# Optimization experiments

Hardware: AMD Instinct MI355X
Metric: run time of the kernel (lower is better)

## Reference

```python
import jax, jax.numpy as jnp
import numpy as np

N, F, H, L = 1536, 32, 64, 3  # num_nodes, num_features, hidden, num_layers
NEG_SLOPE = 0.01
BN_EPS = 1e-5


def _lrelu(x):
    return jnp.where(x >= 0, x, NEG_SLOPE * x)


def _gin_layer(x, src, tgt, eps, w1, b1, w2, b2, g, be):
    # scatter-add aggregation: out[tgt] += x[src] (source_to_target flow)
    agg = jax.ops.segment_sum(x[src], tgt, num_segments=N)
    h = (1.0 + eps) * x + agg
    h = jax.nn.relu(h @ w1 + b1)
    h = jax.nn.relu(h @ w2 + b2)
    # BatchNorm1d, training-mode (batch statistics, biased variance)
    mean = jnp.mean(h, axis=0)
    var = jnp.mean((h - mean) ** 2, axis=0)
    return (h - mean) * jax.lax.rsqrt(var + BN_EPS) * g + be


def setup_inputs() -> dict:
    key = jax.random.key(0)
    ks = iter(jax.random.split(key, 40))

    def rn(shape, scale=0.05):
        return jax.random.normal(next(ks), shape, dtype=jnp.float32) * scale

    inp = {
        "x": rn((N, F), 1.0),
        "node_features": rn((N, F), 1.0),
        # conv1: F -> H
        "c1_eps": jnp.zeros((), jnp.float32),
        "c1_w1": rn((F, H)), "c1_b1": jnp.zeros((H,), jnp.float32),
        "c1_w2": rn((H, H)), "c1_b2": jnp.zeros((H,), jnp.float32),
        "c1_g": jnp.ones((H,), jnp.float32), "c1_be": jnp.zeros((H,), jnp.float32),
        # L-1 additional GIN convs: H -> H (stacked)
        "cv_eps": jnp.zeros((L - 1,), jnp.float32),
        "cv_w1": rn((L - 1, H, H)), "cv_b1": jnp.zeros((L - 1, H), jnp.float32),
        "cv_w2": rn((L - 1, H, H)), "cv_b2": jnp.zeros((L - 1, H), jnp.float32),
        "cv_g": jnp.ones((L - 1, H), jnp.float32), "cv_be": jnp.zeros((L - 1, H), jnp.float32),
        # projection head
        "lin1_w": rn((H, H)), "lin1_b": jnp.zeros((H,), jnp.float32),
        "lin2_w": rn((H, F)), "lin2_b": jnp.zeros((F,), jnp.float32),
        # edge predictor: 2F -> H -> H -> H -> 1
        "ep_w1": rn((2 * F, H)), "ep_b1": jnp.zeros((H,), jnp.float32),
        "ep_w2": rn((H, H)), "ep_b2": jnp.zeros((H,), jnp.float32),
        "ep_w3": rn((H, H)), "ep_b3": jnp.zeros((H,), jnp.float32),
        "ep_w4": rn((H, 1)), "ep_b4": jnp.zeros((1,), jnp.float32),
    }
    return inp


def reference(x, node_features, c1_eps, c1_w1, c1_b1, c1_w2, c1_b2, c1_g, c1_be,
              cv_eps, cv_w1, cv_b1, cv_w2, cv_b2, cv_g, cv_be,
              lin1_w, lin1_b, lin2_w, lin2_b,
              ep_w1, ep_b1, ep_w2, ep_b2, ep_w3, ep_b3, ep_w4, ep_b4):
    # complete-graph upper-triangular edge list (matches torch.combinations order)
    src, tgt = jnp.triu_indices(N, k=1)
    h = node_features  # forward ignores input x
    xinit = h
    h = _lrelu(_gin_layer(h, src, tgt, c1_eps, c1_w1, c1_b1, c1_w2, c1_b2, c1_g, c1_be))
    for i in range(L - 1):
        h = _lrelu(_gin_layer(h, src, tgt, cv_eps[i], cv_w1[i], cv_b1[i],
                              cv_w2[i], cv_b2[i], cv_g[i], cv_be[i]))
    h = _lrelu(h @ lin1_w + lin1_b)
    h = _lrelu(h @ lin2_w + lin2_b)
    h = h + xinit  # [N, F]

    # edge predictor: gather -> MLP -> sigmoid over E edges
    ef = jnp.concatenate([h[src], h[tgt]], axis=-1)  # [E, 2F]
    e = jax.nn.relu(ef @ ep_w1 + ep_b1)
    e = jax.nn.relu(e @ ep_w2 + ep_b2)
    e = jax.nn.relu(e @ ep_w3 + ep_b3)
    e = jax.nn.sigmoid(e @ ep_w4 + ep_b4)[:, 0]  # [E]

    probs = jnp.zeros((N, N), dtype=h.dtype)
    probs = probs.at[src, tgt].set(e).at[tgt, src].set(e)
    return probs
```

## Files before the change

kernel.cpp:

```cpp
#include <hip/hip_runtime.h>
#include <math.h>

#define NN 1536
#define FF 32
#define HH 64
#define EE (NN*(NN-1)/2)
#define EBLK 2493
#define BN_EPS 1e-5f
#define SLOPE 0.01f

typedef _Float16 v8h   __attribute__((ext_vector_type(8)));
typedef __fp16   v2hf  __attribute__((ext_vector_type(2)));
typedef float    f32x4 __attribute__((ext_vector_type(4)));

union V8H { v8h v; v2hf h2[4]; float4 f4; };

__device__ __forceinline__ float lrelu_f(float v){ return v >= 0.f ? v : SLOPE*v; }

__global__ __launch_bounds__(256) void k_first(
    const float* __restrict__ nf, float* __restrict__ H,
    const float* __restrict__ pw2, const float* __restrict__ pw3,
    _Float16* __restrict__ pwf) {
  int bid = blockIdx.x, tid = threadIdx.x;
  if (bid >= 96) {
    int i = (bid - 96)*256 + tid;
    if (i < 8192) {
      int mat = i >> 12, r = i & 4095;
      int k = r >> 6, cout = r & 63;
      int m = cout >> 4, cc = cout & 15;
      int q, g, b;
      if (mat == 0) { q = k >> 5; g = (k >> 3) & 3; b = k & 7; }
      else { int mF = k >> 4; g = (k >> 2) & 3; int rr = k & 3; q = mF >> 1; b = ((mF & 1) << 2) | rr; }
      const float* W = mat ? pw3 : pw2;
      pwf[mat*4096 + ((q*4 + m)*64 + (g*16 + cc))*8 + b] = (_Float16)W[r];
    }
    return;
  }
  __shared__ float part[8][32];
  int c = tid & 31, y = tid >> 5;
  float s = nf[(bid*16 + y)*32 + c] + nf[(bid*16 + y + 8)*32 + c];
  part[y][c] = s;
  __syncthreads();
  if (y == 0) {
    float S = 0.f;
#pragma unroll
    for (int r = 0; r < 8; ++r) S += part[r][c];
    H[bid*64 + c] = S;
  }
}

__global__ __launch_bounds__(256) void k_bn(
    const float* __restrict__ z, const float* __restrict__ P,
    const float* __restrict__ gg, const float* __restrict__ be,
    float* __restrict__ hbuf, float* __restrict__ H) {
  __shared__ float sums[2][128];
  __shared__ float scl[64], sft[64];
  __shared__ float part[4][64];
  int tid = threadIdx.x, bid = blockIdx.x;
  {
    int c2 = tid & 127, half = tid >> 7;
    float S0 = 0.f, S1 = 0.f;
    int j0 = half*48;
    for (int j = j0; j < j0 + 48; j += 2) { S0 += P[j*128 + c2]; S1 += P[(j+1)*128 + c2]; }
    sums[half][c2] = S0 + S1;
  }
  __syncthreads();
  if (tid < 64) {
    float S = sums[0][tid] + sums[1][tid];
    float Q = sums[0][64 + tid] + sums[1][64 + tid];
    float m  = S * (1.f/NN);
    float iv = rsqrtf(Q * (1.f/NN) - m*m + BN_EPS);
    float sc = iv * gg[tid];
    scl[tid] = sc;
    sft[tid] = be[tid] - m*sc;
  }
  __syncthreads();
  int c = tid & 63, y = tid >> 6;
  float sc = scl[c], sh = sft[c];
  float hs = 0.f;
#pragma unroll
  for (int i = 0; i < 4; ++i) {
    int rr = y + 4*i;
    float h = lrelu_f(z[(bid*16 + rr)*64 + c]*sc + sh);
    hbuf[(bid*16 + rr)*64 + c] = h;
    hs += h;
  }
  part[y][c] = hs;
  __syncthreads();
  if (y == 0)
    H[bid*64 + c] = part[0][c] + part[1][c] + part[2][c] + part[3][c];
}

template<int DIN>
__global__ __launch_bounds__(512) void k_mmp(
    const float* __restrict__ hb, const float* __restrict__ H,
    const float* __restrict__ eps_p,
    const float* __restrict__ W1, const float* __restrict__ b1,
    const float* __restrict__ W2, const float* __restrict__ b2,
    float* __restrict__ zout, float* __restrict__ P) {
  __shared__ float W1s[DIN*64];
  __shared__ float W2s[4096];
  __shared__ float red[8][64];
  __shared__ float pf[64];
  __shared__ float hh[16][DIN];
  __shared__ float uls[16*DIN];
  __shared__ float t1s[16][64];
  __shared__ float pp[8][64], pq[8][64];
  int tid = threadIdx.x, bid = blockIdx.x;
  int c = tid & 63, y = tid >> 6;
  for (int i = tid; i < DIN*64; i += 512) W1s[i] = W1[i];
  for (int i = tid; i < 4096; i += 512)   W2s[i] = W2[i];

  {
    float s = 0.f;
    if (c < DIN) for (int j = y; j < bid; j += 8) s += H[j*64 + c];
    red[y][c] = s;
  }
  if (c < DIN) {
    hh[y][c]     = hb[(bid*16 + y)*DIN + c];
    hh[y + 8][c] = hb[(bid*16 + y + 8)*DIN + c];
  }
  __syncthreads();
  if (y == 0 && c < DIN) {
    float S = 0.f;
#pragma unroll
    for (int r = 0; r < 8; ++r) S += red[r][c];
    pf[c] = S;
  }
  __syncthreads();

  float e1 = 1.f + eps_p[0];
  if (c < DIN) {
    for (int rr = y; rr < 16; rr += 8) {
      float run = pf[c];
      for (int r2 = 0; r2 < rr; ++r2) run += hh[r2][c];
      uls[rr*DIN + c] = e1*hh[rr][c] + run;
    }
  }
  __syncthreads();

  float a0 = b1[c], a1 = a0;
  for (int k = 0; k < DIN; ++k) {
    float w = W1s[k*64 + c];
    a0 = fmaf(uls[y*DIN + k],       w, a0);
    a1 = fmaf(uls[(y + 8)*DIN + k], w, a1);
  }
  t1s[y][c]     = fmaxf(a0, 0.f);
  t1s[y + 8][c] = fmaxf(a1, 0.f);
  __syncthreads();

  float z0 = b2[c], z1 = z0;
  for (int k = 0; k < 64; ++k) {
    float w = W2s[k*64 + c];
    z0 = fmaf(t1s[y][k],     w, z0);
    z1 = fmaf(t1s[y + 8][k], w, z1);
  }
  z0 = fmaxf(z0, 0.f); z1 = fmaxf(z1, 0.f);
  zout[(bid*16 + y)*64 + c]     = z0;
  zout[(bid*16 + y + 8)*64 + c] = z1;

  pp[y][c] = z0 + z1;
  pq[y][c] = z0*z0 + z1*z1;
  __syncthreads();
  if (y == 0) {
    float S = 0.f, Q = 0.f;
#pragma unroll
    for (int r = 0; r < 8; ++r) { S += pp[r][c]; Q += pq[r][c]; }
    P[bid*128 + c]      = S;
    P[bid*128 + 64 + c] = Q;
  }
}

__global__ __launch_bounds__(512) void k_head2(
    const float* __restrict__ z, const float* __restrict__ P,
    const float* __restrict__ gg, const float* __restrict__ be,
    const float* __restrict__ l1w, const float* __restrict__ l1b,
    const float* __restrict__ l2w, const float* __restrict__ l2b,
    const float* __restrict__ nf,
    const float* __restrict__ epw1, const float* __restrict__ epb1,
    _Float16* __restrict__ Ah, _Float16* __restrict__ Bh) {
  __shared__ float W1s[4096];
  __shared__ float W2s[2048];
  __shared__ float Was[2048];
  __shared__ float Wbs[2048];
  __shared__ float sums[4][128];
  __shared__ float scratch[4096];
  __shared__ float scl[64], sft[64];
  int tid = threadIdx.x, c = tid & 63, y = tid >> 6;
  for (int i = tid; i < 4096; i += 512) W1s[i] = l1w[i];
  for (int i = tid; i < 2048; i += 512) { W2s[i] = l2w[i]; Was[i] = epw1[i]; Wbs[i] = epw1[2048 + i]; }

  {
    int c2 = tid & 127, q = tid >> 7;
    float S = 0.f;
    for (int j = q*24; j < q*24 + 24; ++j) S += P[j*128 + c2];
    sums[q][c2] = S;
  }
  __syncthreads();
  if (tid < 64) {
    float S = sums[0][tid] + sums[1][tid] + sums[2][tid] + sums[3][tid];
    float Q = sums[0][64+tid] + sums[1][64+tid] + sums[2][64+tid] + sums[3][64+tid];
    float m  = S * (1.f/NN);
    float iv = rsqrtf(Q * (1.f/NN) - m*m + BN_EPS);
    float sc = iv * gg[tid];
    scl[tid] = sc;
    sft[tid] = be[tid] - m*sc;
  }
  __syncthreads();

  float* t0 = scratch;
  float* t1 = scratch + 1024;
  float* t2 = scratch + 2048;
  int r0 = blockIdx.x*16;

  for (int rr = y; rr < 16; rr += 8)
    t0[rr*64 + c] = lrelu_f(z[(r0 + rr)*64 + c]*scl[c] + sft[c]);
  __syncthreads();
  {
    float a0 = l1b[c], a1 = a0;
    for (int k = 0; k < 64; ++k) {
      float w = W1s[k*64 + c];
      a0 = fmaf(t0[y*64 + k],       w, a0);
      a1 = fmaf(t0[(y + 8)*64 + k], w, a1);
    }
    t1[y*64 + c]       = lrelu_f(a0);
    t1[(y + 8)*64 + c] = lrelu_f(a1);
  }
  __syncthreads();
  if (c < 32) {
    float v0 = l2b[c], v1 = v0;
    for (int k = 0; k < 64; ++k) {
      float w = W2s[k*32 + c];
      v0 = fmaf(t1[y*64 + k],       w, v0);
      v1 = fmaf(t1[(y + 8)*64 + k], w, v1);
    }
    t2[y*32 + c]       = lrelu_f(v0) + nf[(r0 + y)*32 + c];
    t2[(y + 8)*32 + c] = lrelu_f(v1) + nf[(r0 + y + 8)*32 + c];
  }
  __syncthreads();
  {
    float av0 = epb1[c], av1 = av0;
    float bv0 = 0.f, bv1 = 0.f;
    for (int k = 0; k < 32; ++k) {
      float wa = Was[k*64 + c], wb = Wbs[k*64 + c];
      av0 = fmaf(t2[y*32 + k], wa, av0);       bv0 = fmaf(t2[y*32 + k], wb, bv0);
      av1 = fmaf(t2[(y + 8)*32 + k], wa, av1); bv1 = fmaf(t2[(y + 8)*32 + k], wb, bv1);
    }
    Ah[(r0 + y)*64 + c]     = (_Float16)av0;  Bh[(r0 + y)*64 + c]     = (_Float16)bv0;
    Ah[(r0 + y + 8)*64 + c] = (_Float16)av1;  Bh[(r0 + y + 8)*64 + c] = (_Float16)bv1;
  }
}

__global__ __launch_bounds__(256, 3) void k_edges_f16(
    const _Float16* __restrict__ Ah, const _Float16* __restrict__ Bh,
    const _Float16* __restrict__ Wf,
    const float* __restrict__ b2, const float* __restrict__ b3,
    const float* __restrict__ w4, const float* __restrict__ b4,
    float* __restrict__ out) {
  __shared__ _Float16 Wl[8192];
  int tid = threadIdx.x, wid = tid >> 6, lane = tid & 63;
  int c = lane & 15, g = lane >> 4;

  {
    const float4* src = (const float4*)Wf;
    float4* dst = (float4*)Wl;
    for (int i = tid; i < 1024; i += 256) dst[i] = src[i];
  }

  int w = blockIdx.x*4 + wid;
  int cum, kk, sbase;
  if (w < 1524) { cum = 0; kk = 12; sbase = 0; }
  else {
    cum = 1524; kk = 11; sbase = 127;
    while (kk > 1 && w >= cum + 128*kk) { cum += 128*kk; sbase += 128; --kk; }
  }
  int idx = w - cum;
  int q = idx / kk;
  int s = sbase + q;
  int t0 = s + 1 + ((idx - q*kk) << 7);

  f32x4 b2v[4], b3v[4];
  v2hf w4h[8];
  int g4 = g*4;
#pragma unroll
  for (int m = 0; m < 4; ++m) {
#pragma unroll
    for (int r = 0; r < 4; ++r) {
      int f = 16*m + g4 + r;
      b2v[m][r] = b2[f]; b3v[m][r] = b3[f];
    }
    v2hf wa = { (__fp16)w4[16*m + g4],     (__fp16)w4[16*m + g4 + 1] };
    v2hf wb = { (__fp16)w4[16*m + g4 + 2], (__fp16)w4[16*m + g4 + 3] };
    w4h[2*m] = wa; w4h[2*m + 1] = wb;
  }
  float b4v = b4[0];

  V8H zu; zu.f4 = make_float4(0.f, 0.f, 0.f, 0.f);
  const v8h vzero = zu.v;
  const v2hf z2 = { (__fp16)0.f, (__fp16)0.f };

  V8H a0, a1;
  a0.f4 = *(const float4*)(Ah + s*64 + g*8);
  a1.f4 = *(const float4*)(Ah + s*64 + 32 + g*8);

  V8H y0a, y1a, y0b, y1b;
  {
    int ta = t0 + c, tb = t0 + 16 + c;
    y0a.f4 = *(const float4*)(Bh + ta*64 + g*8);
    y1a.f4 = *(const float4*)(Bh + ta*64 + 32 + g*8);
    y0b.f4 = *(const float4*)(Bh + tb*64 + g*8);
    y1b.f4 = *(const float4*)(Bh + tb*64 + 32 + g*8);
  }

  const v8h* wl = (const v8h*)Wl;
  __syncthreads();

  for (int it = 0; it < 4; ++it) {
    int tb0 = t0 + (it << 5);
    if (tb0 >= NN) break;
    int ta = tb0 + c, tbx = tb0 + 16 + c;

    V8H f0a, f1a, f0b, f1b;
    f0a.v = __builtin_elementwise_max(a0.v + y0a.v, vzero);
    f1a.v = __builtin_elementwise_max(a1.v + y1a.v, vzero);
    f0b.v = __builtin_elementwise_max(a0.v + y0b.v, vzero);
    f1b.v = __builtin_elementwise_max(a1.v + y1b.v, vzero);

    {
      int tna = tb0 + 32 + c, tnb = tb0 + 48 + c;
      y0a.f4 = *(const float4*)(Bh + tna*64 + g*8);
      y1a.f4 = *(const float4*)(Bh + tna*64 + 32 + g*8);
      y0b.f4 = *(const float4*)(Bh + tnb*64 + g*8);
      y1b.f4 = *(const float4*)(Bh + tnb*64 + 32 + g*8);
    }

    __builtin_amdgcn_s_setprio(1);
    f32x4 acca[4], accb[4];
#pragma unroll
    for (int m = 0; m < 4; ++m) {
      v8h wfrag = wl[m*64 + lane];
      acca[m] = __builtin_amdgcn_mfma_f32_16x16x32_f16(wfrag, f0a.v, b2v[m], 0, 0, 0);
      accb[m] = __builtin_amdgcn_mfma_f32_16x16x32_f16(wfrag, f0b.v, b2v[m], 0, 0, 0);
    }
#pragma unroll
    for (int m = 0; m < 4; ++m) {
      v8h wfrag = wl[(4 + m)*64 + lane];
      acca[m] = __builtin_amdgcn_mfma_f32_16x16x32_f16(wfrag, f1a.v, acca[m], 0, 0, 0);
      accb[m] = __builtin_amdgcn_mfma_f32_16x16x32_f16(wfrag, f1b.v, accb[m], 0, 0, 0);
    }
    __builtin_amdgcn_s_setprio(0);

    V8H p0a, p1a, p0b, p1b;
#pragma unroll
    for (int m = 0; m < 2; ++m) {
      p0a.h2[2*m]     = __builtin_elementwise_max(__builtin_amdgcn_cvt_pkrtz(acca[m][0],   acca[m][1]),   z2);
      p0a.h2[2*m + 1] = __builtin_elementwise_max(__builtin_amdgcn_cvt_pkrtz(acca[m][2],   acca[m][3]),   z2);
      p1a.h2[2*m]     = __builtin_elementwise_max(__builtin_amdgcn_cvt_pkrtz(acca[m+2][0], acca[m+2][1]), z2);
      p1a.h2[2*m + 1] = __builtin_elementwise_max(__builtin_amdgcn_cvt_pkrtz(acca[m+2][2], acca[m+2][3]), z2);
      p0b.h2[2*m]     = __builtin_elementwise_max(__builtin_amdgcn_cvt_pkrtz(accb[m][0],   accb[m][1]),   z2);
      p0b.h2[2*m + 1] = __builtin_elementwise_max(__builtin_amdgcn_cvt_pkrtz(accb[m][2],   accb[m][3]),   z2);
      p1b.h2[2*m]     = __builtin_elementwise_max(__builtin_amdgcn_cvt_pkrtz(accb[m+2][0], accb[m+2][1]), z2);
      p1b.h2[2*m + 1] = __builtin_elementwise_max(__builtin_amdgcn_cvt_pkrtz(accb[m+2][2], accb[m+2][3]), z2);
    }

    __builtin_amdgcn_s_setprio(1);
    f32x4 ac3a[4], ac3b[4];
#pragma unroll
    for (int m = 0; m < 4; ++m) {
      v8h wfrag = wl[512 + m*64 + lane];
      ac3a[m] = __builtin_amdgcn_mfma_f32_16x16x32_f16(wfrag, p0a.v, b3v[m], 0, 0, 0);
      ac3b[m] = __builtin_amdgcn_mfma_f32_16x16x32_f16(wfrag, p0b.v, b3v[m], 0, 0, 0);
    }
#pragma unroll
    for (int m = 0; m < 4; ++m) {
      v8h wfrag = wl[512 + (4 + m)*64 + lane];
      ac3a[m] = __builtin_amdgcn_mfma_f32_16x16x32_f16(wfrag, p1a.v, ac3a[m], 0, 0, 0);
      ac3b[m] = __builtin_amdgcn_mfma_f32_16x16x32_f16(wfrag, p1b.v, ac3b[m], 0, 0, 0);
    }
    __builtin_amdgcn_s_setprio(0);

    float pa = 0.f, pb = 0.f;
#pragma unroll
    for (int m = 0; m < 4; ++m) {
      v2hf la0 = __builtin_elementwise_max(__builtin_amdgcn_cvt_pkrtz(ac3a[m][0], ac3a[m][1]), z2);
      v2hf la1 = __builtin_elementwise_max(__builtin_amdgcn_cvt_pkrtz(ac3a[m][2], ac3a[m][3]), z2);
      v2hf lb0 = __builtin_elementwise_max(__builtin_amdgcn_cvt_pkrtz(ac3b[m][0], ac3b[m][1]), z2);
      v2hf lb1 = __builtin_elementwise_max(__builtin_amdgcn_cvt_pkrtz(ac3b[m][2], ac3b[m][3]), z2);
      pa = __builtin_amdgcn_fdot2(la0, w4h[2*m],     pa, false);
      pa = __builtin_amdgcn_fdot2(la1, w4h[2*m + 1], pa, false);
      pb = __builtin_amdgcn_fdot2(lb0, w4h[2*m],     pb, false);
      pb = __builtin_amdgcn_fdot2(lb1, w4h[2*m + 1], pb, false);
    }
    pa += __shfl_xor(pa, 16, 64);
    pb += __shfl_xor(pb, 16, 64);
    pa += __shfl_xor(pa, 32, 64);
    pb += __shfl_xor(pb, 32, 64);
    float eza = __builtin_amdgcn_exp2f(-1.44269504f * (pa + b4v));
    float ezb = __builtin_amdgcn_exp2f(-1.44269504f * (pb + b4v));
    float proba = __builtin_amdgcn_rcpf(1.f + eza);
    float probb = __builtin_amdgcn_rcpf(1.f + ezb);
    if (lane < 16) {
      if (ta < NN)  out[s*NN + ta]  = proba;
      if (tbx < NN) out[s*NN + tbx] = probb;
    }
  }
}

__global__ __launch_bounds__(256) void k_mirror(float* __restrict__ out) {
  __shared__ float tile[32][33];
  int k = blockIdx.x;
  int bi = (int)((sqrtf(8.f*k + 1.f) - 1.f)*0.5f);
  while (bi*(bi + 1)/2 > k) --bi;
  while ((bi + 1)*(bi + 2)/2 <= k) ++bi;
  int bj = k - bi*(bi + 1)/2;
  int i0 = bi*32, j0 = bj*32;
  int tx = threadIdx.x & 31, ty = threadIdx.x >> 5;
#pragma unroll
  for (int r = 0; r < 4; ++r)
    tile[ty + r*8][tx] = out[(j0 + ty + r*8)*NN + i0 + tx];
  __syncthreads();
#pragma unroll
  for (int r = 0; r < 4; ++r) {
    int row = ty + r*8;
    int i = i0 + row, j = j0 + tx;
    if (bi > bj)      out[i*NN + j] = tile[tx][row];
    else if (i > j)   out[i*NN + j] = tile[tx][row];
    else if (i == j)  out[i*NN + j] = 0.f;
  }
}

extern "C" void kernel_launch(void* const* d_in, const int* in_sizes, int n_in,
                              void* d_out, int out_size, void* d_ws, size_t ws_size,
                              hipStream_t stream) {
  const float* nf     = (const float*)d_in[1];
  const float* c1_eps = (const float*)d_in[2];
  const float* c1_w1  = (const float*)d_in[3];
  const float* c1_b1  = (const float*)d_in[4];
  const float* c1_w2  = (const float*)d_in[5];
  const float* c1_b2  = (const float*)d_in[6];
  const float* c1_g   = (const float*)d_in[7];
  const float* c1_be  = (const float*)d_in[8];
  const float* cv_eps = (const float*)d_in[9];
  const float* cv_w1  = (const float*)d_in[10];
  const float* cv_b1  = (const float*)d_in[11];
  const float* cv_w2  = (const float*)d_in[12];
  const float* cv_b2  = (const float*)d_in[13];
  const float* cv_g   = (const float*)d_in[14];
  const float* cv_be  = (const float*)d_in[15];
  const float* lin1_w = (const float*)d_in[16];
  const float* lin1_b = (const float*)d_in[17];
  const float* lin2_w = (const float*)d_in[18];
  const float* lin2_b = (const float*)d_in[19];
  const float* ep_w1  = (const float*)d_in[20];
  const float* ep_b1  = (const float*)d_in[21];
  const float* ep_w2  = (const float*)d_in[22];
  const float* ep_b2  = (const float*)d_in[23];
  const float* ep_w3  = (const float*)d_in[24];
  const float* ep_b3  = (const float*)d_in[25];
  const float* ep_w4  = (const float*)d_in[26];
  const float* ep_b4  = (const float*)d_in[27];

  float* ws = (float*)d_ws;
  float* zA    = ws;
  float* zB    = zA + NN*64;
  float* hbuf  = zB + NN*64;
  float* H     = hbuf + NN*64;
  float* P     = H + 96*64;
  _Float16* Ah = (_Float16*)(P + 96*128);
  _Float16* Bh = Ah + NN*64;
  _Float16* Wf = Bh + NN*64;

  float* out = (float*)d_out;

  k_first<<<128, 256, 0, stream>>>(nf, H, ep_w2, ep_w3, Wf);
  k_mmp<32><<<96, 512, 0, stream>>>(nf, H, c1_eps, c1_w1, c1_b1, c1_w2, c1_b2, zA, P);

  k_bn<<<96, 256, 0, stream>>>(zA, P, c1_g, c1_be, hbuf, H);
  k_mmp<64><<<96, 512, 0, stream>>>(hbuf, H, cv_eps, cv_w1, cv_b1, cv_w2, cv_b2, zB, P);

  k_bn<<<96, 256, 0, stream>>>(zB, P, cv_g, cv_be, hbuf, H);
  k_mmp<64><<<96, 512, 0, stream>>>(hbuf, H, cv_eps + 1,
      cv_w1 + HH*HH, cv_b1 + HH, cv_w2 + HH*HH, cv_b2 + HH, zA, P);

  k_head2<<<96, 512, 0, stream>>>(zA, P, cv_g + HH, cv_be + HH,
                                  lin1_w, lin1_b, lin2_w, lin2_b, nf,
                                  ep_w1, ep_b1, Ah, Bh);

  k_edges_f16<<<EBLK, 256, 0, stream>>>(Ah, Bh, Wf, ep_b2, ep_b3, ep_w4, ep_b4, out);
  k_mirror<<<1176, 256, 0, stream>>>(out);
}
```

Measured before the change: 83.29 us.

## Compute final edge-MLP dot with MFMA and process two work chunks per wave

```diff
diff --git a/kernel.cpp b/kernel.cpp
--- a/kernel.cpp
+++ b/kernel.cpp
@@ -5,7 +5,7 @@
 #define FF 32
 #define HH 64
 #define EE (NN*(NN-1)/2)
-#define EBLK 2493
+#define EBLK 1248
 #define BN_EPS 1e-5f
 #define SLOPE 0.01f
 
@@ -20,6 +20,7 @@
 __global__ __launch_bounds__(256) void k_first(
     const float* __restrict__ nf, float* __restrict__ H,
     const float* __restrict__ pw2, const float* __restrict__ pw3,
+    const float* __restrict__ pw4,
     _Float16* __restrict__ pwf) {
   int bid = blockIdx.x, tid = threadIdx.x;
   if (bid >= 96) {
@@ -33,6 +34,14 @@
       else { int mF = k >> 4; g = (k >> 2) & 3; int rr = k & 3; q = mF >> 1; b = ((mF & 1) << 2) | rr; }
       const float* W = mat ? pw3 : pw2;
       pwf[mat*4096 + ((q*4 + m)*64 + (g*16 + cc))*8 + b] = (_Float16)W[r];
+    } else if (i < 9216) {
+      int e = i - 8192;
+      int fi = e >> 9, rem = e & 511;
+      int lane = rem >> 3, b = rem & 7;
+      int g = lane >> 4, r = lane & 15;
+      int q = b >> 2, j = b & 3;
+      float val = (r == 0) ? pw4[fi*32 + 16*q + 4*g + j] : 0.f;
+      pwf[i] = (_Float16)val;
     }
     return;
   }
@@ -255,7 +264,7 @@
     const _Float16* __restrict__ Ah, const _Float16* __restrict__ Bh,
     const _Float16* __restrict__ Wf,
     const float* __restrict__ b2, const float* __restrict__ b3,
-    const float* __restrict__ w4, const float* __restrict__ b4,
+    const float* __restrict__ b4,
     float* __restrict__ out) {
   __shared__ _Float16 Wl[8192];
   int tid = threadIdx.x, wid = tid >> 6, lane = tid & 63;
@@ -267,141 +276,149 @@
     for (int i = tid; i < 1024; i += 256) dst[i] = src[i];
   }
 
-  int w = blockIdx.x*4 + wid;
-  int cum, kk, sbase;
-  if (w < 1524) { cum = 0; kk = 12; sbase = 0; }
-  else {
-    cum = 1524; kk = 11; sbase = 127;
-    while (kk > 1 && w >= cum + 128*kk) { cum += 128*kk; sbase += 128; --kk; }
-  }
-  int idx = w - cum;
-  int q = idx / kk;
-  int s = sbase + q;
-  int t0 = s + 1 + ((idx - q*kk) << 7);
-
   f32x4 b2v[4], b3v[4];
-  v2hf w4h[8];
   int g4 = g*4;
 #pragma unroll
-  for (int m = 0; m < 4; ++m) {
+  for (int m = 0; m < 4; ++m)
 #pragma unroll
     for (int r = 0; r < 4; ++r) {
       int f = 16*m + g4 + r;
       b2v[m][r] = b2[f]; b3v[m][r] = b3[f];
     }
-    v2hf wa = { (__fp16)w4[16*m + g4],     (__fp16)w4[16*m + g4 + 1] };
-    v2hf wb = { (__fp16)w4[16*m + g4 + 2], (__fp16)w4[16*m + g4 + 3] };
-    w4h[2*m] = wa; w4h[2*m + 1] = wb;
-  }
   float b4v = b4[0];
+
+  const v8h* wp = (const v8h*)Wf;
+  v8h w4f0 = wp[1024 + lane];
+  v8h w4f1 = wp[1088 + lane];
 
   V8H zu; zu.f4 = make_float4(0.f, 0.f, 0.f, 0.f);
   const v8h vzero = zu.v;
   const v2hf z2 = { (__fp16)0.f, (__fp16)0.f };
-
-  V8H a0, a1;
-  a0.f4 = *(const float4*)(Ah + s*64 + g*8);
-  a1.f4 = *(const float4*)(Ah + s*64 + 32 + g*8);
-
-  V8H y0a, y1a, y0b, y1b;
-  {
-    int ta = t0 + c, tb = t0 + 16 + c;
-    y0a.f4 = *(const float4*)(Bh + ta*64 + g*8);
-    y1a.f4 = *(const float4*)(Bh + ta*64 + 32 + g*8);
-    y0b.f4 = *(const float4*)(Bh + tb*64 + g*8);
-    y1b.f4 = *(const float4*)(Bh + tb*64 + 32 + g*8);
-  }
+  const f32x4 zz = {0.f, 0.f, 0.f, 0.f};
 
   const v8h* wl = (const v8h*)Wl;
   __syncthreads();
 
-  for (int it = 0; it < 4; ++it) {
-    int tb0 = t0 + (it << 5);
-    if (tb0 >= NN) break;
-    int ta = tb0 + c, tbx = tb0 + 16 + c;
-
-    V8H f0a, f1a, f0b, f1b;
-    f0a.v = __builtin_elementwise_max(a0.v + y0a.v, vzero);
-    f1a.v = __builtin_elementwise_max(a1.v + y1a.v, vzero);
-    f0b.v = __builtin_elementwise_max(a0.v + y0b.v, vzero);
-    f1b.v = __builtin_elementwise_max(a1.v + y1b.v, vzero);
-
+  int wbase = (blockIdx.x*4 + wid)*2;
+  for (int ch = 0; ch < 2; ++ch) {
+    int w = wbase + ch;
+
+    int cum, kk, sbase;
+    if (w < 1524) { cum = 0; kk = 12; sbase = 0; }
+    else {
+      cum = 1524; kk = 11; sbase = 127;
+      while (kk > 1 && w >= cum + 128*kk) { cum += 128*kk; sbase += 128; --kk; }
+    }
+    int idx = w - cum;
+    int q = idx / kk;
+    int s = sbase + q;
+    int t0 = s + 1 + ((idx - q*kk) << 7);
+    if (t0 >= NN + 64) continue;
+
+    V8H a0, a1;
+    a0.f4 = *(const float4*)(Ah + s*64 + g*8);
+    a1.f4 = *(const float4*)(Ah + s*64 + 32 + g*8);
+
+    V8H y0a, y1a, y0b, y1b;
     {
-      int tna = tb0 + 32 + c, tnb = tb0 + 48 + c;
-      y0a.f4 = *(const float4*)(Bh + tna*64 + g*8);
-      y1a.f4 = *(const float4*)(Bh + tna*64 + 32 + g*8);
-      y0b.f4 = *(const float4*)(Bh + tnb*64 + g*8);
-      y1b.f4 = *(const float4*)(Bh + tnb*64 + 32 + g*8);
-    }
-
-    __builtin_amdgcn_s_setprio(1);
-    f32x4 acca[4], accb[4];
-#pragma unroll
-    for (int m = 0; m < 4; ++m) {
-      v8h wfrag = wl[m*64 + lane];
-      acca[m] = __builtin_amdgcn_mfma_f32_16x16x32_f16(wfrag, f0a.v, b2v[m], 0, 0, 0);
-      accb[m] = __builtin_amdgcn_mfma_f32_16x16x32_f16(wfrag, f0b.v, b2v[m], 0, 0, 0);
-    }
-#pragma unroll
-    for (int m = 0; m < 4; ++m) {
-      v8h wfrag = wl[(4 + m)*64 + lane];
-      acca[m] = __builtin_amdgcn_mfma_f32_16x16x32_f16(wfrag, f1a.v, acca[m], 0, 0, 0);
-      accb[m] = __builtin_amdgcn_mfma_f32_16x16x32_f16(wfrag, f1b.v, accb[m], 0, 0, 0);
-    }
-    __builtin_amdgcn_s_setprio(0);
-
-    V8H p0a, p1a, p0b, p1b;
-#pragma unroll
-    for (int m = 0; m < 2; ++m) {
-      p0a.h2[2*m]     = __builtin_elementwise_max(__builtin_amdgcn_cvt_pkrtz(acca[m][0],   acca[m][1]),   z2);
-      p0a.h2[2*m + 1] = __builtin_elementwise_max(__builtin_amdgcn_cvt_pkrtz(acca[m][2],   acca[m][3]),   z2);
-      p1a.h2[2*m]     = __builtin_elementwise_max(__builtin_amdgcn_cvt_pkrtz(acca[m+2][0], acca[m+2][1]), z2);
-      p1a.h2[2*m + 1] = __builtin_elementwise_max(__builtin_amdgcn_cvt_pkrtz(acca[m+2][2], acca[m+2][3]), z2);
-      p0b.h2[2*m]     = __builtin_elementwise_max(__builtin_amdgcn_cvt_pkrtz(accb[m][0],   accb[m][1]),   z2);
-      p0b.h2[2*m + 1] = __builtin_elementwise_max(__builtin_amdgcn_cvt_pkrtz(accb[m][2],   accb[m][3]),   z2);
-      p1b.h2[2*m]     = __builtin_elementwise_max(__builtin_amdgcn_cvt_pkrtz(accb[m+2][0], accb[m+2][1]), z2);
-      p1b.h2[2*m + 1] = __builtin_elementwise_max(__builtin_amdgcn_cvt_pkrtz(accb[m+2][2], accb[m+2][3]), z2);
-    }
-
-    __builtin_amdgcn_s_setprio(1);
-    f32x4 ac3a[4], ac3b[4];
-#pragma unroll
-    for (int m = 0; m < 4; ++m) {
-      v8h wfrag = wl[512 + m*64 + lane];
-      ac3a[m] = __builtin_amdgcn_mfma_f32_16x16x32_f16(wfrag, p0a.v, b3v[m], 0, 0, 0);
-      ac3b[m] = __builtin_amdgcn_mfma_f32_16x16x32_f16(wfrag, p0b.v, b3v[m], 0, 0, 0);
-    }
-#pragma unroll
-    for (int m = 0; m < 4; ++m) {
-      v8h wfrag = wl[512 + (4 + m)*64 + lane];
-      ac3a[m] = __builtin_amdgcn_mfma_f32_16x16x32_f16(wfrag, p1a.v, ac3a[m], 0, 0, 0);
-      ac3b[m] = __builtin_amdgcn_mfma_f32_16x16x32_f16(wfrag, p1b.v, ac3b[m], 0, 0, 0);
-    }
-    __builtin_amdgcn_s_setprio(0);
-
-    float pa = 0.f, pb = 0.f;
-#pragma unroll
-    for (int m = 0; m < 4; ++m) {
-      v2hf la0 = __builtin_elementwise_max(__builtin_amdgcn_cvt_pkrtz(ac3a[m][0], ac3a[m][1]), z2);
-      v2hf la1 = __builtin_elementwise_max(__builtin_amdgcn_cvt_pkrtz(ac3a[m][2], ac3a[m][3]), z2);
-      v2hf lb0 = __builtin_elementwise_max(__builtin_amdgcn_cvt_pkrtz(ac3b[m][0], ac3b[m][1]), z2);
-      v2hf lb1 = __builtin_elementwise_max(__builtin_amdgcn_cvt_pkrtz(ac3b[m][2], ac3b[m][3]), z2);
-      pa = __builtin_amdgcn_fdot2(la0, w4h[2*m],     pa, false);
-      pa = __builtin_amdgcn_fdot2(la1, w4h[2*m + 1], pa, false);
-      pb = __builtin_amdgcn_fdot2(lb0, w4h[2*m],     pb, false);
-      pb = __builtin_amdgcn_fdot2(lb1, w4h[2*m + 1], pb, false);
-    }
-    pa += __shfl_xor(pa, 16, 64);
-    pb += __shfl_xor(pb, 16, 64);
-    pa += __shfl_xor(pa, 32, 64);
-    pb += __shfl_xor(pb, 32, 64);
-    float eza = __builtin_amdgcn_exp2f(-1.44269504f * (pa + b4v));
-    float ezb = __builtin_amdgcn_exp2f(-1.44269504f * (pb + b4v));
-    float proba = __builtin_amdgcn_rcpf(1.f + eza);
-    float probb = __builtin_amdgcn_rcpf(1.f + ezb);
-    if (lane < 16) {
-      if (ta < NN)  out[s*NN + ta]  = proba;
-      if (tbx < NN) out[s*NN + tbx] = probb;
+      int ta = t0 + c, tb = t0 + 16 + c;
+      y0a.f4 = *(const float4*)(Bh + ta*64 + g*8);
+      y1a.f4 = *(const float4*)(Bh + ta*64 + 32 + g*8);
+      y0b.f4 = *(const float4*)(Bh + tb*64 + g*8);
+      y1b.f4 = *(const float4*)(Bh + tb*64 + 32 + g*8);
+    }
+
+    for (int it = 0; it < 4; ++it) {
+      int tb0 = t0 + (it << 5);
+      if (tb0 >= NN) break;
+      int ta = tb0 + c, tbx = tb0 + 16 + c;
+
+      V8H f0a, f1a, f0b, f1b;
+      f0a.v = __builtin_elementwise_max(a0.v + y0a.v, vzero);
+      f1a.v = __builtin_elementwise_max(a1.v + y1a.v, vzero);
+      f0b.v = __builtin_elementwise_max(a0.v + y0b.v, vzero);
+      f1b.v = __builtin_elementwise_max(a1.v + y1b.v, vzero);
+
+      {
+        int tna = tb0 + 32 + c, tnb = tb0 + 48 + c;
+        y0a.f4 = *(const float4*)(Bh + tna*64 + g*8);
+        y1a.f4 = *(const float4*)(Bh + tna*64 + 32 + g*8);
+        y0b.f4 = *(const float4*)(Bh + tnb*64 + g*8);
+        y1b.f4 = *(const float4*)(Bh + tnb*64 + 32 + g*8);
+      }
+
+      __builtin_amdgcn_s_setprio(1);
+      f32x4 acca[4], accb[4];
+#pragma unroll
+      for (int m = 0; m < 4; ++m) {
+        v8h wfrag = wl[m*64 + lane];
+        acca[m] = __builtin_amdgcn_mfma_f32_16x16x32_f16(wfrag, f0a.v, b2v[m], 0, 0, 0);
+        accb[m] = __builtin_amdgcn_mfma_f32_16x16x32_f16(wfrag, f0b.v, b2v[m], 0, 0, 0);
+      }
+#pragma unroll
+      for (int m = 0; m < 4; ++m) {
+        v8h wfrag = wl[(4 + m)*64 + lane];
+        acca[m] = __builtin_amdgcn_mfma_f32_16x16x32_f16(wfrag, f1a.v, acca[m], 0, 0, 0);
+        accb[m] = __builtin_amdgcn_mfma_f32_16x16x32_f16(wfrag, f1b.v, accb[m], 0, 0, 0);
+      }
+      __builtin_amdgcn_s_setprio(0);
+
+      V8H p0a, p1a, p0b, p1b;
+#pragma unroll
+      for (int m = 0; m < 2; ++m) {
+        p0a.h2[2*m]     = __builtin_elementwise_max(__builtin_amdgcn_cvt_pkrtz(acca[m][0],   acca[m][1]),   z2);
+        p0a.h2[2*m + 1] = __builtin_elementwise_max(__builtin_amdgcn_cvt_pkrtz(acca[m][2],   acca[m][3]),   z2);
+        p1a.h2[2*m]     = __builtin_elementwise_max(__builtin_amdgcn_cvt_pkrtz(acca[m+2][0], acca[m+2][1]), z2);
+        p1a.h2[2*m + 1] = __builtin_elementwise_max(__builtin_amdgcn_cvt_pkrtz(acca[m+2][2], acca[m+2][3]), z2);
+        p0b.h2[2*m]     = __builtin_elementwise_max(__builtin_amdgcn_cvt_pkrtz(accb[m][0],   accb[m][1]),   z2);
+        p0b.h2[2*m + 1] = __builtin_elementwise_max(__builtin_amdgcn_cvt_pkrtz(accb[m][2],   accb[m][3]),   z2);
+        p1b.h2[2*m]     = __builtin_elementwise_max(__builtin_amdgcn_cvt_pkrtz(accb[m+2][0], accb[m+2][1]), z2);
+        p1b.h2[2*m + 1] = __builtin_elementwise_max(__builtin_amdgcn_cvt_pkrtz(accb[m+2][2], accb[m+2][3]), z2);
+      }
+
+      __builtin_amdgcn_s_setprio(1);
+      f32x4 ac3a[4], ac3b[4];
+#pragma unroll
+      for (int m = 0; m < 4; ++m) {
+        v8h wfrag = wl[512 + m*64 + lane];
+        ac3a[m] = __builtin_amdgcn_mfma_f32_16x16x32_f16(wfrag, p0a.v, b3v[m], 0, 0, 0);
+        ac3b[m] = __builtin_amdgcn_mfma_f32_16x16x32_f16(wfrag, p0b.v, b3v[m], 0, 0, 0);
+      }
+#pragma unroll
+      for (int m = 0; m < 4; ++m) {
+        v8h wfrag = wl[512 + (4 + m)*64 + lane];
+        ac3a[m] = __builtin_amdgcn_mfma_f32_16x16x32_f16(wfrag, p1a.v, ac3a[m], 0, 0, 0);
+        ac3b[m] = __builtin_amdgcn_mfma_f32_16x16x32_f16(wfrag, p1b.v, ac3b[m], 0, 0, 0);
+      }
+      __builtin_amdgcn_s_setprio(0);
+
+      V8H q0a, q1a, q0b, q1b;
+#pragma unroll
+      for (int m = 0; m < 2; ++m) {
+        q0a.h2[2*m]     = __builtin_elementwise_max(__builtin_amdgcn_cvt_pkrtz(ac3a[m][0],   ac3a[m][1]),   z2);
+        q0a.h2[2*m + 1] = __builtin_elementwise_max(__builtin_amdgcn_cvt_pkrtz(ac3a[m][2],   ac3a[m][3]),   z2);
+        q1a.h2[2*m]     = __builtin_elementwise_max(__builtin_amdgcn_cvt_pkrtz(ac3a[m+2][0], ac3a[m+2][1]), z2);
+        q1a.h2[2*m + 1] = __builtin_elementwise_max(__builtin_amdgcn_cvt_pkrtz(ac3a[m+2][2], ac3a[m+2][3]), z2);
+        q0b.h2[2*m]     = __builtin_elementwise_max(__builtin_amdgcn_cvt_pkrtz(ac3b[m][0],   ac3b[m][1]),   z2);
+        q0b.h2[2*m + 1] = __builtin_elementwise_max(__builtin_amdgcn_cvt_pkrtz(ac3b[m][2],   ac3b[m][3]),   z2);
+        q1b.h2[2*m]     = __builtin_elementwise_max(__builtin_amdgcn_cvt_pkrtz(ac3b[m+2][0], ac3b[m+2][1]), z2);
+        q1b.h2[2*m + 1] = __builtin_elementwise_max(__builtin_amdgcn_cvt_pkrtz(ac3b[m+2][2], ac3b[m+2][3]), z2);
+      }
+      __builtin_amdgcn_s_setprio(1);
+      f32x4 da = __builtin_amdgcn_mfma_f32_16x16x32_f16(w4f0, q0a.v, zz, 0, 0, 0);
+      f32x4 db = __builtin_amdgcn_mfma_f32_16x16x32_f16(w4f0, q0b.v, zz, 0, 0, 0);
+      da = __builtin_amdgcn_mfma_f32_16x16x32_f16(w4f1, q1a.v, da, 0, 0, 0);
+      db = __builtin_amdgcn_mfma_f32_16x16x32_f16(w4f1, q1b.v, db, 0, 0, 0);
+      __builtin_amdgcn_s_setprio(0);
+
+      float eza = __builtin_amdgcn_exp2f(-1.44269504f * (da[0] + b4v));
+      float ezb = __builtin_amdgcn_exp2f(-1.44269504f * (db[0] + b4v));
+      float proba = __builtin_amdgcn_rcpf(1.f + eza);
+      float probb = __builtin_amdgcn_rcpf(1.f + ezb);
+      if (lane < 16) {
+        if (ta < NN)  out[s*NN + ta]  = proba;
+        if (tbx < NN) out[s*NN + tbx] = probb;
+      }
     }
   }
 }
@@ -472,7 +489,7 @@
 
   float* out = (float*)d_out;
 
-  k_first<<<128, 256, 0, stream>>>(nf, H, ep_w2, ep_w3, Wf);
+  k_first<<<132, 256, 0, stream>>>(nf, H, ep_w2, ep_w3, ep_w4, Wf);
   k_mmp<32><<<96, 512, 0, stream>>>(nf, H, c1_eps, c1_w1, c1_b1, c1_w2, c1_b2, zA, P);
 
   k_bn<<<96, 256, 0, stream>>>(zA, P, c1_g, c1_be, hbuf, H);
@@ -486,6 +503,6 @@
                                   lin1_w, lin1_b, lin2_w, lin2_b, nf,
                                   ep_w1, ep_b1, Ah, Bh);
 
-  k_edges_f16<<<EBLK, 256, 0, stream>>>(Ah, Bh, Wf, ep_b2, ep_b3, ep_w4, ep_b4, out);
+  k_edges_f16<<<EBLK, 256, 0, stream>>>(Ah, Bh, Wf, ep_b2, ep_b3, ep_b4, out);
   k_mirror<<<1176, 256, 0, stream>>>(out);
 }
```

Result: faster. 81.31 us (-2.4%).
